# Kernel tuning notes

Hardware: AMD Instinct MI355X
Metric: run time of the kernel (lower is better)

## Reference

```python
import jax, jax.numpy as jnp
import numpy as np

B, S, HID = 1, 2048, 4096
H, KH, D = 32, 8, 128          # query heads, kv heads, head_dim
ROT = 64                       # rotary_dim = head_dim * partial_rotary_factor (0.5)
THETA = 10000.0
EPS = 1e-5
SCALE = D ** -0.5
NEG = -1e30


def setup_inputs() -> dict:
    key = jax.random.key(0)
    ks = jax.random.split(key, 7)
    return {
        "hidden_states": jax.random.normal(ks[0], (B, S, HID), jnp.float32),
        "Wq": jax.random.normal(ks[1], (H * D, HID), jnp.float32) * 0.02,
        "Wk": jax.random.normal(ks[2], (KH * D, HID), jnp.float32) * 0.02,
        "Wv": jax.random.normal(ks[3], (KH * D, HID), jnp.float32) * 0.02,
        "Wo": jax.random.normal(ks[4], (H * D, HID), jnp.float32).T.reshape(HID, H * D) * 0.02,
        "q_norm_w": jax.random.uniform(ks[5], (D,), jnp.float32),
        "k_norm_w": jax.random.uniform(ks[6], (D,), jnp.float32),
        "position_ids": jnp.arange(S, dtype=jnp.int32)[None, :],
    }


def rms_norm(x, w):
    # per-head RMSNorm in fp32, scale by (weight + 1)
    xf = x.astype(jnp.float32)
    var = jnp.mean(xf * xf, axis=-1, keepdims=True)
    return (xf * jax.lax.rsqrt(var + EPS) * (w.astype(jnp.float32) + 1.0)).astype(x.dtype)


def rope_cos_sin(position_ids):
    inv_freq = 1.0 / (THETA ** (jnp.arange(0, ROT, 2, dtype=jnp.float32) / ROT))
    freqs = position_ids.astype(jnp.float32)[..., None] * inv_freq  # [B,S,ROT/2]
    emb = jnp.concatenate([freqs, freqs], axis=-1)                  # [B,S,ROT]
    return jnp.cos(emb)[:, None], jnp.sin(emb)[:, None]             # [B,1,S,ROT]


def rotate_half(x):
    x1, x2 = jnp.split(x, 2, axis=-1)
    return jnp.concatenate([-x2, x1], axis=-1)


def apply_partial_rope(x, cos, sin):
    x_rot, x_pass = x[..., :ROT], x[..., ROT:]
    x_rot = x_rot * cos + rotate_half(x_rot) * sin
    return jnp.concatenate([x_rot, x_pass], axis=-1)


def reference(hidden_states, Wq, Wk, Wv, Wo, q_norm_w, k_norm_w, position_ids):
    # projections -> [B, heads, S, D]
    q = (hidden_states @ Wq.T).reshape(B, S, H, D).transpose(0, 2, 1, 3)
    k = (hidden_states @ Wk.T).reshape(B, S, KH, D).transpose(0, 2, 1, 3)
    v = (hidden_states @ Wv.T).reshape(B, S, KH, D).transpose(0, 2, 1, 3)

    q = rms_norm(q, q_norm_w)
    k = rms_norm(k, k_norm_w)

    cos, sin = rope_cos_sin(position_ids)
    q = apply_partial_rope(q, cos, sin)
    k = apply_partial_rope(k, cos, sin)

    # repeat kv heads (GQA) -> [B, H, S, D]
    rep = H // KH
    k = jnp.broadcast_to(k[:, :, None], (B, KH, rep, S, D)).reshape(B, H, S, D)
    v = jnp.broadcast_to(v[:, :, None], (B, KH, rep, S, D)).reshape(B, H, S, D)

    scores = jnp.einsum("bhqd,bhkd->bhqk", q, k) * SCALE
    causal = jnp.tril(jnp.ones((S, S), bool))
    scores = jnp.where(causal, scores, NEG)
    attn = jax.nn.softmax(scores, axis=-1)
    out = jnp.einsum("bhqk,bhkd->bhqd", attn, v)        # [B,H,S,D]
    out = out.transpose(0, 2, 1, 3).reshape(B, S, H * D)
    return out @ Wo.T                                    # [B,S,HID]
```

## Files before the change

### kernel.cpp

```cpp
#include <hip/hip_runtime.h>
#include <hip/hip_bf16.h>

#define AS1 __attribute__((address_space(1)))
#define AS3 __attribute__((address_space(3)))

typedef __attribute__((ext_vector_type(8))) short short8;
typedef __attribute__((ext_vector_type(4))) short short4v;
typedef __attribute__((ext_vector_type(4))) float f32x4;

constexpr int S_ = 2048;
constexpr int HID_ = 4096;
constexpr int NH = 32;
constexpr int NKH = 8;
constexpr float EPS_ = 1e-5f;
constexpr float SCALE_ = 0.08838834764831845f;

__device__ __forceinline__ short f2bf(float f) {
  __hip_bfloat16 h = __float2bfloat16(f);
  return *reinterpret_cast<short*>(&h);
}

__global__ __launch_bounds__(256) void cast_bf16_kernel(const float4* __restrict__ src,
                                                        short4v* __restrict__ dst, int n4) {
  int i = blockIdx.x * 256 + threadIdx.x;
  if (i >= n4) return;
  float4 v = src[i];
  short4v o;
  o[0] = f2bf(v.x); o[1] = f2bf(v.y); o[2] = f2bf(v.z); o[3] = f2bf(v.w);
  dst[i] = o;
}

__global__ __launch_bounds__(256) void gemm_bt(const short* __restrict__ A,
                                               const short* __restrict__ B,
                                               float* __restrict__ C,
                                               int M, int N, int K) {
  __shared__ __align__(16) short As[128 * 32];
  __shared__ __align__(16) short Bs[128 * 32];
  const int t = threadIdx.x, w = t >> 6, lane = t & 63;
  const int m0 = blockIdx.y * 128, n0 = blockIdx.x * 128;
  const int wr = w >> 1, wc = w & 1;
  const int l15 = lane & 15, lk = (lane >> 4) * 8;
  f32x4 acc[4][4];
#pragma unroll
  for (int a = 0; a < 4; ++a)
#pragma unroll
    for (int b = 0; b < 4; ++b) acc[a][b] = (f32x4){0.f, 0.f, 0.f, 0.f};

  const int c0 = (w * 2) * 64 + lane;
  const int c1 = c0 + 64;
  const int rA0 = c0 >> 2, kc0 = (c0 & 3) * 8;
  const int rA1 = c1 >> 2, kc1 = (c1 & 3) * 8;

  for (int k0 = 0; k0 < K; k0 += 32) {
    __builtin_amdgcn_global_load_lds((const AS1 void*)(A + (long)(m0 + rA0) * K + k0 + kc0),
                                     (AS3 void*)(As + (w * 2) * 512), 16, 0, 0);
    __builtin_amdgcn_global_load_lds((const AS1 void*)(A + (long)(m0 + rA1) * K + k0 + kc1),
                                     (AS3 void*)(As + (w * 2 + 1) * 512), 16, 0, 0);
    __builtin_amdgcn_global_load_lds((const AS1 void*)(B + (long)(n0 + rA0) * K + k0 + kc0),
                                     (AS3 void*)(Bs + (w * 2) * 512), 16, 0, 0);
    __builtin_amdgcn_global_load_lds((const AS1 void*)(B + (long)(n0 + rA1) * K + k0 + kc1),
                                     (AS3 void*)(Bs + (w * 2 + 1) * 512), 16, 0, 0);
    __syncthreads();
    short8 af[4], bfr[4];
#pragma unroll
    for (int mi = 0; mi < 4; ++mi)
      af[mi] = *(const short8*)(As + (wr * 64 + mi * 16 + l15) * 32 + lk);
#pragma unroll
    for (int ni = 0; ni < 4; ++ni)
      bfr[ni] = *(const short8*)(Bs + (wc * 64 + ni * 16 + l15) * 32 + lk);
#pragma unroll
    for (int mi = 0; mi < 4; ++mi)
#pragma unroll
      for (int ni = 0; ni < 4; ++ni)
        acc[mi][ni] = __builtin_amdgcn_mfma_f32_16x16x32_bf16(af[mi], bfr[ni], acc[mi][ni], 0, 0, 0);
    __syncthreads();
  }
#pragma unroll
  for (int mi = 0; mi < 4; ++mi)
#pragma unroll
    for (int ni = 0; ni < 4; ++ni)
#pragma unroll
      for (int r = 0; r < 4; ++r) {
        int m = m0 + wr * 64 + mi * 16 + (lane >> 4) * 4 + r;
        int n = n0 + wc * 64 + ni * 16 + l15;
        C[(long)m * N + n] = acc[mi][ni][r];
      }
}

__global__ __launch_bounds__(256) void normrope_kernel(const float* __restrict__ QKV,
    const int* __restrict__ pos_ids, const float* __restrict__ qw,
    const float* __restrict__ kw,
    short* __restrict__ Qn, short* __restrict__ Kn) {
  const int lane = threadIdx.x & 63;
  const long row = (long)blockIdx.x * 4 + (threadIdx.x >> 6);
  const long NQ = (long)S_ * NH;
  const float* src;
  short* dst;
  const float* wv;
  int s;
  float scl = 1.f;
  if (row < NQ) {
    s = (int)(row >> 5); int h = (int)(row & 31);
    src = QKV + (long)s * 6144 + h * 128;
    dst = Qn + ((long)h * S_ + s) * 128;
    wv = qw; scl = SCALE_;
  } else {
    long r2 = row - NQ; s = (int)(r2 >> 3); int kh = (int)(r2 & 7);
    src = QKV + (long)s * 6144 + 4096 + kh * 128;
    dst = Kn + ((long)kh * S_ + s) * 128;
    wv = kw;
  }
  float x0 = src[lane], x1 = src[lane + 64];
  float ss = x0 * x0 + x1 * x1;
#pragma unroll
  for (int m = 1; m < 64; m <<= 1) ss += __shfl_xor(ss, m);
  float inv = rsqrtf(ss * (1.f / 128.f) + EPS_);
  x0 = x0 * inv * (wv[lane] + 1.f);
  x1 = x1 * inv * (wv[lane + 64] + 1.f);
  int pos = pos_ids[s];
  int i = lane & 31;
  float invf = expf(-logf(10000.f) * ((float)(2 * i) / 64.f));
  float f = (float)pos * invf;
  float c = cosf(f), sn = sinf(f);
  float p = __shfl_xor(x0, 32);
  x0 = (lane < 32) ? (x0 * c - p * sn) : (x0 * c + p * sn);
  dst[lane] = f2bf(x0 * scl);
  dst[lane + 64] = f2bf(x1 * scl);
}

__global__ __launch_bounds__(256) void vtrans_kernel(const float* __restrict__ QKV,
                                                     short* __restrict__ Vt) {
  __shared__ __align__(16) float lt[64][68];
  const int t = threadIdx.x;
  const int s0 = blockIdx.x * 64, d0 = blockIdx.y * 64, kh = blockIdx.z;
  const float* src = QKV + (long)s0 * 6144 + 5120 + kh * 128 + d0;
#pragma unroll
  for (int i = 0; i < 4; ++i) {
    int idx = t + i * 256;
    int r = idx >> 4, c4 = (idx & 15) * 4;
    float4 v = *(const float4*)(src + (long)r * 6144 + c4);
    *(float4*)&lt[r][c4] = v;
  }
  __syncthreads();
  int d = t >> 2, seg = (t & 3) * 16;
  short* dst = Vt + ((long)kh * 128 + d0 + d) * S_ + s0 + seg;
  short8 a, b2;
#pragma unroll
  for (int j = 0; j < 8; ++j) a[j] = f2bf(lt[seg + j][d]);
#pragma unroll
  for (int j = 0; j < 8; ++j) b2[j] = f2bf(lt[seg + 8 + j][d]);
  *(short8*)dst = a;
  *(short8*)(dst + 8) = b2;
}

__global__ __launch_bounds__(512, 2) void attn_kernel(const short* __restrict__ Qn,
    const short* __restrict__ Kn, const short* __restrict__ Vt,
    short* __restrict__ O) {
  __shared__ __align__(16) short Ks[64 * 128];
  __shared__ __align__(16) short Vs[128 * 64];
  __shared__ __align__(16) short Ps[8][16 * 64];
  const int t = threadIdx.x, w = t >> 6, lane = t & 63;
  const int b = blockIdx.x;
  const int h = b & 31, qt = 15 - (b >> 5);
  const int kh = h >> 2;
  const int q0 = qt * 128;
  const int l15 = lane & 15, lk = (lane >> 4) * 8;

  short8 qf[4];
  {
    const short* Qh = Qn + ((long)h * S_ + q0 + w * 16) * 128;
#pragma unroll
    for (int ks = 0; ks < 4; ++ks)
      qf[ks] = *(const short8*)(Qh + l15 * 128 + ks * 32 + lk);
  }
  f32x4 o[8];
#pragma unroll
  for (int nf = 0; nf < 8; ++nf) o[nf] = (f32x4){0.f, 0.f, 0.f, 0.f};
  float mrun[4], lrun[4];
#pragma unroll
  for (int r = 0; r < 4; ++r) { mrun[r] = -1e30f; lrun[r] = 0.f; }

  const short* Khp = Kn + (long)kh * S_ * 128;
  const short* Vtp = Vt + (long)kh * 128 * S_;

  const int krr = w * 8 + (lane >> 4);
  const int kc = lane & 15;
  const int vdd = w * 16 + (lane >> 3);
  const int vc = lane & 7;
  char* pw = (char*)Ps[w];
  const int mrow = (lane >> 4) * 4;

  for (int kv0 = 0; kv0 < q0 + 128; kv0 += 64) {
#pragma unroll
    for (int j = 0; j < 2; ++j) {
      int rr = krr + j * 4;
      __builtin_amdgcn_global_load_lds(
          (const AS1 void*)(Khp + (long)(kv0 + rr) * 128 + ((kc ^ (rr & 7)) * 8)),
          (AS3 void*)(Ks + (w * 8 + j * 4) * 128 + lane * 8), 16, 0, 0);
    }
#pragma unroll
    for (int j = 0; j < 2; ++j) {
      int d = vdd + j * 8;
      __builtin_amdgcn_global_load_lds(
          (const AS1 void*)(Vtp + (long)d * S_ + kv0 + ((vc ^ (d & 7)) * 8)),
          (AS3 void*)(Vs + (w * 16 + j * 8) * 64 + lane * 8), 16, 0, 0);
    }
    __syncthreads();

    const bool active = (kv0 <= q0 + w * 16 + 15);
    if (active) {
      f32x4 sc[4];
#pragma unroll
      for (int ni = 0; ni < 4; ++ni) sc[ni] = (f32x4){0.f, 0.f, 0.f, 0.f};
#pragma unroll
      for (int ks = 0; ks < 4; ++ks)
#pragma unroll
        for (int ni = 0; ni < 4; ++ni) {
          int row = ni * 16 + l15;
          int bb = row * 256 + (ks * 32 + lk) * 2; bb ^= (row & 7) << 4;
          short8 kf = *(const short8*)((const char*)Ks + bb);
          sc[ni] = __builtin_amdgcn_mfma_f32_16x16x32_bf16(qf[ks], kf, sc[ni], 0, 0, 0);
        }
      if (kv0 + 64 > q0 + w * 16) {
#pragma unroll
        for (int ni = 0; ni < 4; ++ni)
#pragma unroll
          for (int r = 0; r < 4; ++r) {
            int qm = q0 + w * 16 + mrow + r;
            int kcol = kv0 + ni * 16 + l15;
            if (kcol > qm) sc[ni][r] = -1e30f;
          }
      }
      short pb[4][4];
#pragma unroll
      for (int r = 0; r < 4; ++r) {
        float mx = fmaxf(fmaxf(sc[0][r], sc[1][r]), fmaxf(sc[2][r], sc[3][r]));
        mx = fmaxf(mx, __shfl_xor(mx, 1));
        mx = fmaxf(mx, __shfl_xor(mx, 2));
        mx = fmaxf(mx, __shfl_xor(mx, 4));
        mx = fmaxf(mx, __shfl_xor(mx, 8));
        float mnew = fmaxf(mrun[r], mx);
        float scale = expf(mrun[r] - mnew);
        mrun[r] = mnew;
        float ssum = 0.f;
#pragma unroll
        for (int ni = 0; ni < 4; ++ni) {
          float p = expf(sc[ni][r] - mnew);
          ssum += p;
          pb[ni][r] = f2bf(p);
        }
        ssum += __shfl_xor(ssum, 1);
        ssum += __shfl_xor(ssum, 2);
        ssum += __shfl_xor(ssum, 4);
        ssum += __shfl_xor(ssum, 8);
        lrun[r] = lrun[r] * scale + ssum;
#pragma unroll
        for (int nf = 0; nf < 8; ++nf) o[nf][r] *= scale;
      }
#pragma unroll
      for (int ni = 0; ni < 4; ++ni)
#pragma unroll
        for (int r = 0; r < 4; ++r) {
          int m = mrow + r;
          int bb = m * 128 + (ni * 16 + l15) * 2; bb ^= (m & 7) << 4;
          *(short*)(pw + bb) = pb[ni][r];
        }
#pragma unroll
      for (int ks2 = 0; ks2 < 2; ++ks2) {
        int bp = l15 * 128 + (ks2 * 32 + lk) * 2; bp ^= (l15 & 7) << 4;
        short8 pf = *(const short8*)(pw + bp);
#pragma unroll
        for (int nf = 0; nf < 8; ++nf) {
          int bv = (nf * 16 + l15) * 128 + (ks2 * 32 + lk) * 2; bv ^= (l15 & 7) << 4;
          short8 vf = *(const short8*)((const char*)Vs + bv);
          o[nf] = __builtin_amdgcn_mfma_f32_16x16x32_bf16(pf, vf, o[nf], 0, 0, 0);
        }
      }
    }
    __syncthreads();
  }
#pragma unroll
  for (int r = 0; r < 4; ++r) {
    float invl = 1.f / lrun[r];
    int m = q0 + w * 16 + mrow + r;
#pragma unroll
    for (int nf = 0; nf < 8; ++nf)
      O[(long)m * 4096 + h * 128 + nf * 16 + l15] = f2bf(o[nf][r] * invl);
  }
}

extern "C" void kernel_launch(void* const* d_in, const int* in_sizes, int n_in,
                              void* d_out, int out_size, void* d_ws, size_t ws_size,
                              hipStream_t stream) {
  const float* hidden = (const float*)d_in[0];
  const float* Wq = (const float*)d_in[1];
  const float* Wk = (const float*)d_in[2];
  const float* Wv = (const float*)d_in[3];
  const float* Wo = (const float*)d_in[4];
  const float* qw = (const float*)d_in[5];
  const float* kw = (const float*)d_in[6];
  const int* pos = (const int*)d_in[7];
  float* out = (float*)d_out;

  char* ws = (char*)d_ws;
  short* hid_bf  = (short*)(ws + 0);
  short* Wqkv_bf = (short*)(ws + 16777216L);
  short* Wo_bf   = (short*)(ws + 67108864L);
  float* QKVf    = (float*)(ws + 100663296L);
  short* Qn      = (short*)(ws + 150994944L);
  short* Kn      = (short*)(ws + 167772160L);
  short* Vt      = (short*)(ws + 171966464L);
  short* AO      = hid_bf;

  auto cast = [&](const float* s_, short* d_, long n) {
    int n4 = (int)(n / 4);
    cast_bf16_kernel<<<(n4 + 255) / 256, 256, 0, stream>>>((const float4*)s_, (short4v*)d_, n4);
  };
  cast(hidden, hid_bf, (long)S_ * HID_);
  cast(Wq, Wqkv_bf, (long)4096 * 4096);
  cast(Wk, Wqkv_bf + (long)4096 * 4096, (long)1024 * 4096);
  cast(Wv, Wqkv_bf + (long)5120 * 4096, (long)1024 * 4096);
  cast(Wo, Wo_bf, (long)4096 * 4096);

  gemm_bt<<<dim3(6144 / 128, S_ / 128), 256, 0, stream>>>(hid_bf, Wqkv_bf, QKVf, S_, 6144, HID_);

  normrope_kernel<<<(S_ * (NH + NKH)) / 4, 256, 0, stream>>>(QKVf, pos, qw, kw, Qn, Kn);

  vtrans_kernel<<<dim3(S_ / 64, 2, NKH), 256, 0, stream>>>(QKVf, Vt);

  attn_kernel<<<dim3(512), 512, 0, stream>>>(Qn, Kn, Vt, AO);

  gemm_bt<<<dim3(HID_ / 128, S_ / 128), 256, 0, stream>>>(AO, Wo_bf, out, S_, HID_, HID_);
}
```

Before: 599.2 us.

## Replace GEMM with 256x256-tile, 8-wave, double-buffered swizzled-LDS pipelined kernel

Replaces the simple 128x128 single-buffer GEMM with a 256x256-tile kernel using 8 waves, 64-wide K steps, and a double-buffered 128KB dynamic LDS. Global-to-LDS loads are issued in quarter-stages interleaved with MFMA phases, using manual vmcnt waits, barriers and setprio. An XOR swizzle on the LDS layout is meant to avoid bank conflicts, and an XCD-aware block remap is meant to improve L2 locality. The goal is to overlap memory with compute and raise data reuse, at the cost of much fewer blocks (192/128), which underfills the CUs, and fragile hand-written synchronisation.

New measurement: 602.8 us. About the same (+0.6%).

```diff
diff --git a/kernel.cpp b/kernel.cpp
--- a/kernel.cpp
+++ b/kernel.cpp
@@ -30,60 +30,132 @@
   dst[i] = o;
 }
 
-__global__ __launch_bounds__(256) void gemm_bt(const short* __restrict__ A,
-                                               const short* __restrict__ B,
-                                               float* __restrict__ C,
-                                               int M, int N, int K) {
-  __shared__ __align__(16) short As[128 * 32];
-  __shared__ __align__(16) short Bs[128 * 32];
+__global__ __launch_bounds__(512, 2) void gemm8_bt(const short* __restrict__ A,
+                                                   const short* __restrict__ B,
+                                                   float* __restrict__ C,
+                                                   int M, int N, int K) {
+  extern __shared__ __align__(16) char smem[];
   const int t = threadIdx.x, w = t >> 6, lane = t & 63;
-  const int m0 = blockIdx.y * 128, n0 = blockIdx.x * 128;
-  const int wr = w >> 1, wc = w & 1;
-  const int l15 = lane & 15, lk = (lane >> 4) * 8;
-  f32x4 acc[4][4];
-#pragma unroll
-  for (int a = 0; a < 4; ++a)
-#pragma unroll
-    for (int b = 0; b < 4; ++b) acc[a][b] = (f32x4){0.f, 0.f, 0.f, 0.f};
-
-  const int c0 = (w * 2) * 64 + lane;
-  const int c1 = c0 + 64;
-  const int rA0 = c0 >> 2, kc0 = (c0 & 3) * 8;
-  const int rA1 = c1 >> 2, kc1 = (c1 & 3) * 8;
-
-  for (int k0 = 0; k0 < K; k0 += 32) {
-    __builtin_amdgcn_global_load_lds((const AS1 void*)(A + (long)(m0 + rA0) * K + k0 + kc0),
-                                     (AS3 void*)(As + (w * 2) * 512), 16, 0, 0);
-    __builtin_amdgcn_global_load_lds((const AS1 void*)(A + (long)(m0 + rA1) * K + k0 + kc1),
-                                     (AS3 void*)(As + (w * 2 + 1) * 512), 16, 0, 0);
-    __builtin_amdgcn_global_load_lds((const AS1 void*)(B + (long)(n0 + rA0) * K + k0 + kc0),
-                                     (AS3 void*)(Bs + (w * 2) * 512), 16, 0, 0);
-    __builtin_amdgcn_global_load_lds((const AS1 void*)(B + (long)(n0 + rA1) * K + k0 + kc1),
-                                     (AS3 void*)(Bs + (w * 2 + 1) * 512), 16, 0, 0);
-    __syncthreads();
-    short8 af[4], bfr[4];
-#pragma unroll
-    for (int mi = 0; mi < 4; ++mi)
-      af[mi] = *(const short8*)(As + (wr * 64 + mi * 16 + l15) * 32 + lk);
-#pragma unroll
-    for (int ni = 0; ni < 4; ++ni)
-      bfr[ni] = *(const short8*)(Bs + (wc * 64 + ni * 16 + l15) * 32 + lk);
-#pragma unroll
-    for (int mi = 0; mi < 4; ++mi)
-#pragma unroll
-      for (int ni = 0; ni < 4; ++ni)
-        acc[mi][ni] = __builtin_amdgcn_mfma_f32_16x16x32_bf16(af[mi], bfr[ni], acc[mi][ni], 0, 0, 0);
-    __syncthreads();
-  }
-#pragma unroll
-  for (int mi = 0; mi < 4; ++mi)
-#pragma unroll
-    for (int ni = 0; ni < 4; ++ni)
+  const int nbx = N >> 8;
+  int wg = blockIdx.x;
+  const int cpx = gridDim.x >> 3;
+  wg = (wg & 7) * cpx + (wg >> 3);
+  const int by = wg / nbx, bx = wg % nbx;
+  const long m0 = (long)by << 8, n0 = (long)bx << 8;
+  const int wr = w >> 2, wc = w & 3;
+  const int l15 = lane & 15, l4 = lane >> 4;
+  const int NT = K >> 6;
+
+  f32x4 acc[8][4];
+#pragma unroll
+  for (int f = 0; f < 8; ++f)
+#pragma unroll
+    for (int g = 0; g < 4; ++g) acc[f][g] = (f32x4){0.f, 0.f, 0.f, 0.f};
+
+  auto STAGE = [&](int h) {
+    int hm = h & (4 * NT - 1);
+    int tt = hm >> 2, half = hm & 3;
+    int buf = tt & 1;
+    long k0 = (long)tt << 6;
+    const short* src = (half < 2) ? A : B;
+    long r0 = (half < 2) ? m0 : n0;
+    char* lbase = smem + buf * 65536 + ((half >> 1) << 15) + ((half & 1) << 14);
+#pragma unroll
+    for (int j = 0; j < 2; ++j) {
+      int row = ((half & 1) << 7) + j * 64 + w * 8 + (lane >> 3);
+      int cs = (lane & 7) ^ (((row >> 2) & 1) << 1);
+      __builtin_amdgcn_global_load_lds(
+          (const AS1 void*)(src + (r0 + row) * K + k0 + cs * 8),
+          (AS3 void*)(lbase + j * 8192 + w * 1024 + lane * 16), 16, 0, 0);
+    }
+  };
+  auto LDA = [&](int buf, int f, int s) -> short8 {
+    int ra = wr * 128 + f * 16 + l15;
+    int byte = (ra * 128 + s * 64 + l4 * 16) ^ (((ra >> 2) & 1) << 5);
+    return *(const short8*)(smem + buf * 65536 + byte);
+  };
+  auto LDB = [&](int buf, int g, int s) -> short8 {
+    int rb = wc * 64 + g * 16 + l15;
+    int byte = (rb * 128 + s * 64 + l4 * 16) ^ (((rb >> 2) & 1) << 5);
+    return *(const short8*)(smem + buf * 65536 + 32768 + byte);
+  };
+
+#pragma unroll
+  for (int h = 0; h < 8; ++h) STAGE(h);
+  asm volatile("s_waitcnt vmcnt(8)" ::: "memory");
+  asm volatile("s_barrier" ::: "memory");
+
+  short8 af[4][2], bf2[4][2];
+  for (int tt = 0; tt < NT; ++tt) {
+    const int buf = tt & 1;
+    const int p = tt * 4;
+#pragma unroll
+    for (int f = 0; f < 4; ++f) { af[f][0] = LDA(buf, f, 0); af[f][1] = LDA(buf, f, 1); }
+#pragma unroll
+    for (int g = 0; g < 2; ++g) { bf2[g][0] = LDB(buf, g, 0); bf2[g][1] = LDB(buf, g, 1); }
+    if (tt) STAGE(p + 5);
+    asm volatile("s_barrier" ::: "memory");
+    __builtin_amdgcn_s_setprio(1);
+#pragma unroll
+    for (int f = 0; f < 4; ++f)
+#pragma unroll
+      for (int g = 0; g < 2; ++g) {
+        acc[f][g] = __builtin_amdgcn_mfma_f32_16x16x32_bf16(af[f][0], bf2[g][0], acc[f][g], 0, 0, 0);
+        acc[f][g] = __builtin_amdgcn_mfma_f32_16x16x32_bf16(af[f][1], bf2[g][1], acc[f][g], 0, 0, 0);
+      }
+    __builtin_amdgcn_s_setprio(0);
+    asm volatile("s_barrier" ::: "memory");
+#pragma unroll
+    for (int g = 0; g < 2; ++g) { bf2[2 + g][0] = LDB(buf, 2 + g, 0); bf2[2 + g][1] = LDB(buf, 2 + g, 1); }
+    if (tt) STAGE(p + 6);
+    asm volatile("s_barrier" ::: "memory");
+    __builtin_amdgcn_s_setprio(1);
+#pragma unroll
+    for (int f = 0; f < 4; ++f)
+#pragma unroll
+      for (int g = 0; g < 2; ++g) {
+        acc[f][2 + g] = __builtin_amdgcn_mfma_f32_16x16x32_bf16(af[f][0], bf2[2 + g][0], acc[f][2 + g], 0, 0, 0);
+        acc[f][2 + g] = __builtin_amdgcn_mfma_f32_16x16x32_bf16(af[f][1], bf2[2 + g][1], acc[f][2 + g], 0, 0, 0);
+      }
+    __builtin_amdgcn_s_setprio(0);
+    asm volatile("s_barrier" ::: "memory");
+#pragma unroll
+    for (int f = 0; f < 4; ++f) { af[f][0] = LDA(buf, 4 + f, 0); af[f][1] = LDA(buf, 4 + f, 1); }
+    if (tt) STAGE(p + 7);
+    asm volatile("s_barrier" ::: "memory");
+    __builtin_amdgcn_s_setprio(1);
+#pragma unroll
+    for (int f = 0; f < 4; ++f)
+#pragma unroll
+      for (int g = 0; g < 2; ++g) {
+        acc[4 + f][g] = __builtin_amdgcn_mfma_f32_16x16x32_bf16(af[f][0], bf2[g][0], acc[4 + f][g], 0, 0, 0);
+        acc[4 + f][g] = __builtin_amdgcn_mfma_f32_16x16x32_bf16(af[f][1], bf2[g][1], acc[4 + f][g], 0, 0, 0);
+      }
+    __builtin_amdgcn_s_setprio(0);
+    asm volatile("s_barrier" ::: "memory");
+    STAGE(p + 8);
+    asm volatile("s_barrier" ::: "memory");
+    __builtin_amdgcn_s_setprio(1);
+#pragma unroll
+    for (int f = 0; f < 4; ++f)
+#pragma unroll
+      for (int g = 0; g < 2; ++g) {
+        acc[4 + f][2 + g] = __builtin_amdgcn_mfma_f32_16x16x32_bf16(af[f][0], bf2[2 + g][0], acc[4 + f][2 + g], 0, 0, 0);
+        acc[4 + f][2 + g] = __builtin_amdgcn_mfma_f32_16x16x32_bf16(af[f][1], bf2[2 + g][1], acc[4 + f][2 + g], 0, 0, 0);
+      }
+    __builtin_amdgcn_s_setprio(0);
+    asm volatile("s_waitcnt vmcnt(2)" ::: "memory");
+    asm volatile("s_barrier" ::: "memory");
+  }
+#pragma unroll
+  for (int f = 0; f < 8; ++f)
+#pragma unroll
+    for (int g = 0; g < 4; ++g)
 #pragma unroll
       for (int r = 0; r < 4; ++r) {
-        int m = m0 + wr * 64 + mi * 16 + (lane >> 4) * 4 + r;
-        int n = n0 + wc * 64 + ni * 16 + l15;
-        C[(long)m * N + n] = acc[mi][ni][r];
+        long m = m0 + wr * 128 + f * 16 + l4 * 4 + r;
+        long n = n0 + wc * 64 + g * 16 + l15;
+        C[m * N + n] = acc[f][g][r];
       }
 }
 
@@ -312,6 +384,9 @@
   short* Vt      = (short*)(ws + 171966464L);
   short* AO      = hid_bf;
 
+  (void)hipFuncSetAttribute((const void*)gemm8_bt,
+                            hipFuncAttributeMaxDynamicSharedMemorySize, 131072);
+
   auto cast = [&](const float* s_, short* d_, long n) {
     int n4 = (int)(n / 4);
     cast_bf16_kernel<<<(n4 + 255) / 256, 256, 0, stream>>>((const float4*)s_, (short4v*)d_, n4);
@@ -322,13 +397,11 @@
   cast(Wv, Wqkv_bf + (long)5120 * 4096, (long)1024 * 4096);
   cast(Wo, Wo_bf, (long)4096 * 4096);
 
-  gemm_bt<<<dim3(6144 / 128, S_ / 128), 256, 0, stream>>>(hid_bf, Wqkv_bf, QKVf, S_, 6144, HID_);
+  gemm8_bt<<<dim3(192), 512, 131072, stream>>>(hid_bf, Wqkv_bf, QKVf, S_, 6144, HID_);
 
   normrope_kernel<<<(S_ * (NH + NKH)) / 4, 256, 0, stream>>>(QKVf, pos, qw, kw, Qn, Kn);
-
   vtrans_kernel<<<dim3(S_ / 64, 2, NKH), 256, 0, stream>>>(QKVf, Vt);
-
   attn_kernel<<<dim3(512), 512, 0, stream>>>(Qn, Kn, Vt, AO);
 
-  gemm_bt<<<dim3(HID_ / 128, S_ / 128), 256, 0, stream>>>(AO, Wo_bf, out, S_, HID_, HID_);
-}
+  gemm8_bt<<<dim3(128), 512, 131072, stream>>>(AO, Wo_bf, out, S_, HID_, HID_);
+}
```
